# Kernel optimization log

Hardware: AMD Instinct MI355X
Metric: run time of the kernel (lower is better)

The kernel has to match this reference:

```python
import jax, jax.numpy as jnp
import numpy as np

N_NODES = 50000
N_EDGES = 600000
N_GRAPHS = 64
HID = 128
NLAYERS = 4
IN_DIM = 5
NCLS = 5
EPS = 1e-5


def setup_inputs() -> dict:
    key = jax.random.key(0)
    ks = jax.random.split(key, 16)
    x = jax.random.normal(ks[0], (N_NODES, IN_DIM), dtype=jnp.float32)
    edge_index = jax.random.randint(ks[1], (2, N_EDGES), 0, N_NODES, dtype=jnp.int64)
    batch = jnp.sort(jax.random.randint(ks[2], (N_NODES,), 0, N_GRAPHS, dtype=jnp.int64))
    s = 0.05
    Wp = jax.random.normal(ks[3], (IN_DIM, HID), jnp.float32) * s
    bp = jnp.zeros((HID,), jnp.float32)
    Wg = jax.random.normal(ks[4], (NLAYERS, HID, HID), jnp.float32) * s
    bg = jnp.zeros((NLAYERS, HID), jnp.float32)
    gamma = jnp.ones((NLAYERS, HID), jnp.float32)
    beta = jnp.zeros((NLAYERS, HID), jnp.float32)
    W1 = jax.random.normal(ks[5], (2 * HID, HID), jnp.float32) * s
    b1 = jnp.zeros((HID,), jnp.float32)
    W2 = jax.random.normal(ks[6], (HID, HID // 2), jnp.float32) * s
    b2 = jnp.zeros((HID // 2,), jnp.float32)
    W3 = jax.random.normal(ks[7], (HID // 2, NCLS), jnp.float32) * s
    b3 = jnp.zeros((NCLS,), jnp.float32)
    return {"x": x, "edge_index": edge_index, "batch": batch, "Wp": Wp, "bp": bp,
            "Wg": Wg, "bg": bg, "gamma": gamma, "beta": beta,
            "W1": W1, "b1": b1, "W2": W2, "b2": b2, "W3": W3, "b3": b3}


def reference(x, edge_index, batch, Wp, bp, Wg, bg, gamma, beta, W1, b1, W2, b2, W3, b3):
    N = x.shape[0]
    # GCN with added self-loops and symmetric normalization (PyG GCNConv defaults)
    loop = jnp.arange(N)
    src = jnp.concatenate([edge_index[0], loop])
    dst = jnp.concatenate([edge_index[1], loop])
    deg = jax.ops.segment_sum(jnp.ones_like(dst, dtype=x.dtype), dst, num_segments=N)
    dinv = jax.lax.rsqrt(deg)  # deg >= 1 thanks to self-loops
    norm = dinv[src] * dinv[dst]  # [E+N]
    h = x @ Wp + bp  # [N, HID]
    for i in range(NLAYERS):
        m = h @ Wg[i]
        agg = jax.ops.segment_sum(m[src] * norm[:, None], dst, num_segments=N) + bg[i]
        # BatchNorm1d (training-mode stats over nodes)
        mu = jnp.mean(agg, axis=0)
        var = jnp.var(agg, axis=0)
        h = gamma[i] * (agg - mu) * jax.lax.rsqrt(var + EPS) + beta[i]
        h = jax.nn.relu(h)  # dropout is identity in eval mode
    # mean_max global pooling per graph
    cnt = jax.ops.segment_sum(jnp.ones((N,), h.dtype), batch, num_segments=N_GRAPHS)
    x_mean = jax.ops.segment_sum(h, batch, num_segments=N_GRAPHS) / jnp.maximum(cnt, 1.0)[:, None]
    x_max = jax.ops.segment_max(h, batch, num_segments=N_GRAPHS)
    x_max = jnp.where(jnp.isfinite(x_max), x_max, 0.0)
    pooled = jnp.concatenate([x_mean, x_max], axis=1)  # [B, 2*HID]
    h1 = jax.nn.relu(pooled @ W1 + b1)
    h2 = jax.nn.relu(h1 @ W2 + b2)
    return h2 @ W3 + b3  # [B, num_classes]
```

## Files before the change

### kernel.cpp

```cpp
#include <hip/hip_runtime.h>
#include <hip/hip_bf16.h>

#define N_NODES 50000
#define N_EDGES 600000
#define N_GRAPHS 64
#define HID 128
#define NLAYERS 4
#define IN_DIM 5
#define NCLS 5
#define EPS 1e-5f
#define SCAN_BLK ((N_NODES + 511) / 512)
#define POOL_CHUNKS 16
#define BSLOT 64
#define WS 136

typedef __attribute__((ext_vector_type(8))) short s16x8;
typedef __attribute__((ext_vector_type(4))) float f32x4;

__device__ __forceinline__ unsigned short f2bf(float x) {
    unsigned u = __float_as_uint(x);
    unsigned r = (u + 0x7fffu + ((u >> 16) & 1u)) >> 16;
    return (unsigned short)r;
}
__device__ __forceinline__ float2 bfpair(unsigned u) {
    float2 r;
    r.x = __uint_as_float(u << 16);
    r.y = __uint_as_float(u & 0xffff0000u);
    return r;
}
__device__ __forceinline__ float bf2f(unsigned short s) {
    return __uint_as_float(((unsigned)s) << 16);
}


__global__ void k_count(const int* __restrict__ dst, int* __restrict__ cnt) {
    int i = blockIdx.x * blockDim.x + threadIdx.x;
    if (i < N_EDGES) atomicAdd(&cnt[dst[i]], 1);
}

__global__ void k_scan1(const int* __restrict__ cnt, int* __restrict__ rp, int* __restrict__ bsum) {
    __shared__ int s[512];
    int t = threadIdx.x;
    int i = blockIdx.x * 512 + t;
    int v = (i < N_NODES) ? cnt[i] : 0;
    s[t] = v;
    __syncthreads();
    for (int off = 1; off < 512; off <<= 1) {
        int x = (t >= off) ? s[t - off] : 0;
        __syncthreads();
        s[t] += x;
        __syncthreads();
    }
    if (i < N_NODES) rp[i + 1] = s[t];
    if (t == 511) bsum[blockIdx.x] = s[511];
}

__global__ void k_scan2g(int* __restrict__ bsum, const int* __restrict__ batch,
                         int* __restrict__ gstart) {
    if (blockIdx.x == 0) {
        __shared__ int s[128];
        int t = threadIdx.x;
        int v = (t < SCAN_BLK) ? bsum[t] : 0;
        s[t] = v;
        __syncthreads();
        for (int off = 1; off < 128; off <<= 1) {
            int x = (t >= off) ? s[t - off] : 0;
            __syncthreads();
            s[t] += x;
            __syncthreads();
        }
        if (t < SCAN_BLK) bsum[t] = s[t] - v;
    } else {
        int t = threadIdx.x;
        if (t <= N_GRAPHS) {
            int lo = 0, hi = N_NODES;
            while (lo < hi) {
                int mid = (lo + hi) >> 1;
                if (batch[mid] < t) lo = mid + 1; else hi = mid;
            }
            gstart[t] = lo;
        }
    }
}

__global__ void k_scan3d(int* __restrict__ rp, const int* __restrict__ bsum,
                         const int* __restrict__ cnt, float* __restrict__ dinv) {
    int i = blockIdx.x * 512 + threadIdx.x;
    if (i < N_NODES) {
        rp[i + 1] += bsum[blockIdx.x];
        dinv[i] = rsqrtf((float)(cnt[i] + 1));
    }
    if (i == 0) rp[0] = 0;
}

__global__ void k_fill(const int* __restrict__ src, const int* __restrict__ dst,
                       const int* __restrict__ rp, int* __restrict__ cursor,
                       int2* __restrict__ cw, const float* __restrict__ dinv) {
    int e = blockIdx.x * blockDim.x + threadIdx.x;
    if (e < N_EDGES) {
        int d = dst[e];
        int pos = atomicAdd(&cursor[d], 1);
        int s = src[e];
        int2 p;
        p.x = s;
        p.y = __float_as_int(dinv[s]);
        cw[rp[d] + pos] = p;
    }
}


__global__ __launch_bounds__(256) void k_gemmM(const unsigned short* __restrict__ Abf,
                                               const float* __restrict__ x,
                                               const float* __restrict__ Wp,
                                               const float* __restrict__ bp,
                                               const float* __restrict__ W,
                                               unsigned short* __restrict__ Bm,
                                               const float* __restrict__ scale,
                                               const float* __restrict__ shift,
                                               int layer0) {
    __shared__ unsigned short Wt[HID * WS];
    __shared__ unsigned short Al[64 * WS];
    __shared__ float Wpl[IN_DIM * HID];
    __shared__ float bpl[HID];
    __shared__ float xl[64 * IN_DIM];
    int t = threadIdx.x;
    for (int idx = t; idx < HID * HID; idx += 256) {
        int k = idx >> 7, n = idx & 127;
        Wt[n * WS + k] = f2bf(W[idx]);
    }
    if (layer0) {
        for (int idx = t; idx < IN_DIM * HID; idx += 256) Wpl[idx] = Wp[idx];
        if (t < HID) bpl[t] = bp[t];
    }
    int lane = t & 63, wv = t >> 6;
    int rbase = (wv & 1) * 32;
    int cbase = (wv >> 1) * 64;
    int mr = lane & 15, q = lane >> 4;
    const int numTiles = (N_NODES + 63) / 64;
    for (int tile = blockIdx.x; tile < numTiles; tile += gridDim.x) {
        int n0 = tile * 64;
        __syncthreads();
        if (layer0) {
            for (int idx = t; idx < 64 * IN_DIM; idx += 256) {
                int g = n0 * IN_DIM + idx;
                xl[idx] = (g < N_NODES * IN_DIM) ? x[g] : 0.f;
            }
            __syncthreads();
            for (int idx = t; idx < 64 * HID; idx += 256) {
                int n = idx >> 7, k = idx & 127;
                float acc = bpl[k];
#pragma unroll
                for (int j = 0; j < IN_DIM; j++) acc += xl[n * IN_DIM + j] * Wpl[j * HID + k];
                Al[n * WS + k] = f2bf(acc);
            }
        } else {
            const uint2* Ag = (const uint2*)(Abf + (size_t)n0 * HID);
            int limRow = min(64, N_NODES - n0);
            for (int idx = t; idx < 64 * 32; idx += 256) {
                int row = idx >> 5, c4 = idx & 31;
                uint2 u = (row < limRow) ? Ag[row * 32 + c4] : make_uint2(0u, 0u);
                float2 ab = bfpair(u.x);
                float2 cd = bfpair(u.y);
                int kf = c4 * 4;
                float4 sc = *(const float4*)&scale[kf];
                float4 sh = *(const float4*)&shift[kf];
                float v0 = fmaxf(ab.x * sc.x + sh.x, 0.f);
                float v1 = fmaxf(ab.y * sc.y + sh.y, 0.f);
                float v2 = fmaxf(cd.x * sc.z + sh.z, 0.f);
                float v3 = fmaxf(cd.y * sc.w + sh.w, 0.f);
                unsigned lo = (unsigned)f2bf(v0) | ((unsigned)f2bf(v1) << 16);
                unsigned hi = (unsigned)f2bf(v2) | ((unsigned)f2bf(v3) << 16);
                *(uint2*)&Al[row * WS + kf] = make_uint2(lo, hi);
            }
        }
        __syncthreads();
        f32x4 acc[2][4];
#pragma unroll
        for (int rt = 0; rt < 2; rt++)
#pragma unroll
            for (int ct = 0; ct < 4; ct++) acc[rt][ct] = (f32x4){0.f, 0.f, 0.f, 0.f};
#pragma unroll
        for (int kk = 0; kk < HID; kk += 32) {
            s16x8 a0 = *(const s16x8*)&Al[(rbase + mr) * WS + kk + q * 8];
            s16x8 a1 = *(const s16x8*)&Al[(rbase + 16 + mr) * WS + kk + q * 8];
#pragma unroll
            for (int ct = 0; ct < 4; ct++) {
                s16x8 b = *(const s16x8*)&Wt[(cbase + ct * 16 + mr) * WS + kk + q * 8];
                acc[0][ct] = __builtin_amdgcn_mfma_f32_16x16x32_bf16(a0, b, acc[0][ct], 0, 0, 0);
                acc[1][ct] = __builtin_amdgcn_mfma_f32_16x16x32_bf16(a1, b, acc[1][ct], 0, 0, 0);
            }
        }
#pragma unroll
        for (int rt = 0; rt < 2; rt++)
#pragma unroll
            for (int ct = 0; ct < 4; ct++)
#pragma unroll
                for (int r = 0; r < 4; r++) {
                    int node = n0 + rbase + rt * 16 + q * 4 + r;
                    if (node < N_NODES) {
                        int f = cbase + ct * 16 + mr;
                        Bm[(size_t)node * HID + f] = f2bf(acc[rt][ct][r]);
                    }
                }
    }
}


__global__ __launch_bounds__(256) void k_gather(const uint2* __restrict__ Bm2,
                                                const int* __restrict__ rp,
                                                const int2* __restrict__ cw,
                                                const float* __restrict__ dinv,
                                                const float* __restrict__ bg,
                                                unsigned short* __restrict__ Aout,
                                                float* __restrict__ psum,
                                                float* __restrict__ psq) {
    __shared__ float ls[4 * HID], lq[4 * HID];
    int wave = threadIdx.x >> 6;
    int lane = threadIdx.x & 63;
    int s = lane & 31;
    int p = lane >> 5;
    int v = blockIdx.x * 4 + wave;
    int beg = rp[v], end = rp[v + 1];
    float dv = dinv[v];
    float4 acc = make_float4(0.f, 0.f, 0.f, 0.f);
    if (p == 0) {
        uint2 u = Bm2[(size_t)v * 32 + s];
        float2 lo = bfpair(u.x), hi = bfpair(u.y);
        acc.x = lo.x * dv; acc.y = lo.y * dv; acc.z = hi.x * dv; acc.w = hi.y * dv;
    }
    int e = beg + p;
    for (; e + 2 < end; e += 4) {
        int2 pe0 = cw[e];
        int2 pe1 = cw[e + 2];
        uint2 u0 = Bm2[(size_t)pe0.x * 32 + s];
        uint2 u1 = Bm2[(size_t)pe1.x * 32 + s];
        float w0 = __int_as_float(pe0.y);
        float w1 = __int_as_float(pe1.y);
        float2 l0 = bfpair(u0.x), h0 = bfpair(u0.y);
        float2 l1 = bfpair(u1.x), h1 = bfpair(u1.y);
        acc.x += l0.x * w0 + l1.x * w1;
        acc.y += l0.y * w0 + l1.y * w1;
        acc.z += h0.x * w0 + h1.x * w1;
        acc.w += h0.y * w0 + h1.y * w1;
    }
    if (e < end) {
        int2 pe = cw[e];
        uint2 u = Bm2[(size_t)pe.x * 32 + s];
        float w = __int_as_float(pe.y);
        float2 lo = bfpair(u.x), hi = bfpair(u.y);
        acc.x += lo.x * w; acc.y += lo.y * w; acc.z += hi.x * w; acc.w += hi.y * w;
    }
    acc.x += __shfl_xor(acc.x, 32);
    acc.y += __shfl_xor(acc.y, 32);
    acc.z += __shfl_xor(acc.z, 32);
    acc.w += __shfl_xor(acc.w, 32);
    int f = s * 4;
    if (p == 0) {
        float4 bgv = *(const float4*)&bg[f];
        ushort4 o;
        o.x = f2bf(acc.x * dv + bgv.x);
        o.y = f2bf(acc.y * dv + bgv.y);
        o.z = f2bf(acc.z * dv + bgv.z);
        o.w = f2bf(acc.w * dv + bgv.w);
        *(ushort4*)&Aout[(size_t)v * HID + f] = o;
        float vx = bf2f(o.x), vy = bf2f(o.y), vz = bf2f(o.z), vw = bf2f(o.w);
        ls[wave * HID + f + 0] = vx;
        ls[wave * HID + f + 1] = vy;
        ls[wave * HID + f + 2] = vz;
        ls[wave * HID + f + 3] = vw;
        lq[wave * HID + f + 0] = vx * vx;
        lq[wave * HID + f + 1] = vy * vy;
        lq[wave * HID + f + 2] = vz * vz;
        lq[wave * HID + f + 3] = vw * vw;
    }
    __syncthreads();
    int tt = threadIdx.x;
    if (tt < HID) {
        float ssum = ls[tt] + ls[HID + tt] + ls[2 * HID + tt] + ls[3 * HID + tt];
        float ssq = lq[tt] + lq[HID + tt] + lq[2 * HID + tt] + lq[3 * HID + tt];
        int slot = blockIdx.x & (BSLOT - 1);
        atomicAdd(&psum[slot * HID + tt], ssum);
        atomicAdd(&psq[slot * HID + tt], ssq);
    }
}


__global__ __launch_bounds__(128) void k_bnfin(float* __restrict__ psum,
                                               float* __restrict__ psq,
                                               const float* __restrict__ gamma,
                                               const float* __restrict__ beta,
                                               float* __restrict__ scale,
                                               float* __restrict__ shift) {
    int f = threadIdx.x;
    float s = 0.f, s2 = 0.f;
#pragma unroll 8
    for (int b = 0; b < BSLOT; b++) {
        s += psum[b * HID + f];
        s2 += psq[b * HID + f];
    }
#pragma unroll 8
    for (int b = 0; b < BSLOT; b++) {
        psum[b * HID + f] = 0.f;
        psq[b * HID + f] = 0.f;
    }
    const float invN = 1.f / (float)N_NODES;
    float mu = s * invN;
    float var = s2 * invN - mu * mu;
    float rs = rsqrtf(var + EPS) * gamma[f];
    scale[f] = rs;
    shift[f] = beta[f] - mu * rs;
}


__global__ __launch_bounds__(128) void k_pool(const unsigned short* __restrict__ A,
                                              const float* __restrict__ scale,
                                              const float* __restrict__ shift,
                                              const int* __restrict__ gstart,
                                              float* __restrict__ poolPart) {
    int g = blockIdx.x;
    int c = blockIdx.y;
    int f = threadIdx.x;
    int beg = gstart[g], end = gstart[g + 1];
    int len = end - beg;
    int per = (len + POOL_CHUNKS - 1) / POOL_CHUNKS;
    int s0 = beg + c * per;
    int s1 = min(s0 + per, end);
    float sc = scale[f], sh = shift[f];
    float sa = 0.f, sb = 0.f, ma = 0.f, mb = 0.f;
    int n = s0;
    for (; n + 1 < s1; n += 2) {
        float v0 = bf2f(A[(size_t)n * HID + f]);
        float v1 = bf2f(A[(size_t)(n + 1) * HID + f]);
        v0 = fmaxf(v0 * sc + sh, 0.f);
        v1 = fmaxf(v1 * sc + sh, 0.f);
        sa += v0; ma = fmaxf(ma, v0);
        sb += v1; mb = fmaxf(mb, v1);
    }
    if (n < s1) {
        float v = fmaxf(bf2f(A[(size_t)n * HID + f]) * sc + sh, 0.f);
        sa += v; ma = fmaxf(ma, v);
    }
    poolPart[((size_t)g * POOL_CHUNKS + c) * 256 + f] = sa + sb;
    poolPart[((size_t)g * POOL_CHUNKS + c) * 256 + 128 + f] = fmaxf(ma, mb);
}


__global__ __launch_bounds__(128) void k_head(const float* __restrict__ poolPart,
                                              const int* __restrict__ gstart,
                                              const float* __restrict__ W1, const float* __restrict__ b1,
                                              const float* __restrict__ W2, const float* __restrict__ b2,
                                              const float* __restrict__ W3, const float* __restrict__ b3,
                                              float* __restrict__ out) {
    __shared__ float pl[2 * HID];
    __shared__ float h1[HID];
    __shared__ float h2[HID / 2];
    int g = blockIdx.x, t = threadIdx.x;
    float cnt = fmaxf((float)(gstart[g + 1] - gstart[g]), 1.f);
    float s = 0.f, mx = 0.f;
#pragma unroll
    for (int c = 0; c < POOL_CHUNKS; c++) {
        const float* p = &poolPart[((size_t)g * POOL_CHUNKS + c) * 256];
        s += p[t];
        mx = fmaxf(mx, p[128 + t]);
    }
    pl[t] = s / cnt;
    pl[HID + t] = mx;
    __syncthreads();
    float acc = b1[t];
    for (int k = 0; k < 2 * HID; k++) acc += pl[k] * W1[k * HID + t];
    h1[t] = fmaxf(acc, 0.f);
    __syncthreads();
    if (t < HID / 2) {
        float a2 = b2[t];
        for (int k = 0; k < HID; k++) a2 += h1[k] * W2[k * (HID / 2) + t];
        h2[t] = fmaxf(a2, 0.f);
    }
    __syncthreads();
    if (t < NCLS) {
        float a3 = b3[t];
        for (int k = 0; k < HID / 2; k++) a3 += h2[k] * W3[k * NCLS + t];
        out[g * NCLS + t] = a3;
    }
}

extern "C" void kernel_launch(void* const* d_in, const int* in_sizes, int n_in,
                              void* d_out, int out_size, void* d_ws, size_t ws_size,
                              hipStream_t stream) {
    const float* x     = (const float*)d_in[0];
    const int*   ei    = (const int*)d_in[1];
    const int*   batch = (const int*)d_in[2];
    const float* Wp    = (const float*)d_in[3];
    const float* bp    = (const float*)d_in[4];
    const float* Wg    = (const float*)d_in[5];
    const float* bg    = (const float*)d_in[6];
    const float* gamma = (const float*)d_in[7];
    const float* beta  = (const float*)d_in[8];
    const float* W1    = (const float*)d_in[9];
    const float* b1    = (const float*)d_in[10];
    const float* W2    = (const float*)d_in[11];
    const float* b2    = (const float*)d_in[12];
    const float* W3    = (const float*)d_in[13];
    const float* b3    = (const float*)d_in[14];
    const int* src = ei;
    const int* dst = ei + N_EDGES;
    float* out = (float*)d_out;

    char* base = (char*)d_ws;
    size_t off = 0;
    auto alloc = [&](size_t bytes) -> void* {
        void* p = base + off;
        off += (bytes + 255) & ~(size_t)255;
        return p;
    };
    int*   counts = (int*)alloc((size_t)N_NODES * 4);
    int*   cursor = (int*)alloc((size_t)N_NODES * 4);
    float* psum   = (float*)alloc((size_t)BSLOT * HID * 4);
    float* psq    = (float*)alloc((size_t)BSLOT * HID * 4);
    size_t zeroBytes = off;
    int*   rp      = (int*)alloc((size_t)(N_NODES + 1) * 4);
    int*   bsum    = (int*)alloc(128 * 4);
    int2*  cw      = (int2*)alloc((size_t)N_EDGES * 8);
    float* dinv    = (float*)alloc((size_t)N_NODES * 4);
    float* scaleA  = (float*)alloc((size_t)NLAYERS * HID * 4);
    float* shiftA  = (float*)alloc((size_t)NLAYERS * HID * 4);
    int*   gstart  = (int*)alloc((size_t)(N_GRAPHS + 1) * 4);
    float* poolPart= (float*)alloc((size_t)N_GRAPHS * POOL_CHUNKS * 256 * 4);
    unsigned short* A = (unsigned short*)alloc((size_t)N_NODES * HID * 2);
    unsigned short* B = (unsigned short*)alloc((size_t)N_NODES * HID * 2);
    (void)ws_size; (void)in_sizes; (void)n_in; (void)out_size;

    hipMemsetAsync(d_ws, 0, zeroBytes, stream);

    k_count<<<(N_EDGES + 255) / 256, 256, 0, stream>>>(dst, counts);
    k_scan1<<<SCAN_BLK, 512, 0, stream>>>(counts, rp, bsum);
    k_scan2g<<<2, 128, 0, stream>>>(bsum, batch, gstart);
    k_scan3d<<<SCAN_BLK, 512, 0, stream>>>(rp, bsum, counts, dinv);
    k_fill<<<(N_EDGES + 255) / 256, 256, 0, stream>>>(src, dst, rp, cursor, cw, dinv);

    for (int i = 0; i < NLAYERS; i++) {
        k_gemmM<<<768, 256, 0, stream>>>(A, x, Wp, bp, Wg + (size_t)i * HID * HID, B,
                                         scaleA + ((i == 0) ? 0 : (i - 1)) * HID,
                                         shiftA + ((i == 0) ? 0 : (i - 1)) * HID,
                                         (i == 0) ? 1 : 0);
        k_gather<<<N_NODES / 4, 256, 0, stream>>>((const uint2*)B, rp, cw, dinv,
                                                  bg + i * HID, A, psum, psq);
        k_bnfin<<<1, 128, 0, stream>>>(psum, psq, gamma + i * HID, beta + i * HID,
                                       scaleA + i * HID, shiftA + i * HID);
    }
    dim3 pg(N_GRAPHS, POOL_CHUNKS);
    k_pool<<<pg, 128, 0, stream>>>(A, scaleA + 3 * HID, shiftA + 3 * HID, gstart, poolPart);
    k_head<<<N_GRAPHS, 128, 0, stream>>>(poolPart, gstart, W1, b1, W2, b2, W3, b3, out);
}
```

Measured before the change: 435.5 us.

## Fold BN finalize into consumers and widen gather loads to 16 bytes

```diff
diff --git a/kernel.cpp b/kernel.cpp
--- a/kernel.cpp
+++ b/kernel.cpp
@@ -115,11 +115,14 @@
                                                const float* __restrict__ bp,
                                                const float* __restrict__ W,
                                                unsigned short* __restrict__ Bm,
-                                               const float* __restrict__ scale,
-                                               const float* __restrict__ shift,
+                                               const float* __restrict__ psum,
+                                               const float* __restrict__ psq,
+                                               const float* __restrict__ gamma,
+                                               const float* __restrict__ beta,
                                                int layer0) {
     __shared__ unsigned short Wt[HID * WS];
     __shared__ unsigned short Al[64 * WS];
+    __shared__ float scl[HID], shf[HID];
     __shared__ float Wpl[IN_DIM * HID];
     __shared__ float bpl[HID];
     __shared__ float xl[64 * IN_DIM];
@@ -131,6 +134,19 @@
     if (layer0) {
         for (int idx = t; idx < IN_DIM * HID; idx += 256) Wpl[idx] = Wp[idx];
         if (t < HID) bpl[t] = bp[t];
+    } else if (t < HID) {
+        float s = 0.f, s2 = 0.f;
+#pragma unroll 8
+        for (int b = 0; b < BSLOT; b++) {
+            s += psum[b * HID + t];
+            s2 += psq[b * HID + t];
+        }
+        const float invN = 1.f / (float)N_NODES;
+        float mu = s * invN;
+        float var = s2 * invN - mu * mu;
+        float rs = rsqrtf(var + EPS) * gamma[t];
+        scl[t] = rs;
+        shf[t] = beta[t] - mu * rs;
     }
     int lane = t & 63, wv = t >> 6;
     int rbase = (wv & 1) * 32;
@@ -162,8 +178,8 @@
                 float2 ab = bfpair(u.x);
                 float2 cd = bfpair(u.y);
                 int kf = c4 * 4;
-                float4 sc = *(const float4*)&scale[kf];
-                float4 sh = *(const float4*)&shift[kf];
+                float4 sc = *(const float4*)&scl[kf];
+                float4 sh = *(const float4*)&shf[kf];
                 float v0 = fmaxf(ab.x * sc.x + sh.x, 0.f);
                 float v1 = fmaxf(ab.y * sc.y + sh.y, 0.f);
                 float v2 = fmaxf(cd.x * sc.z + sh.z, 0.f);
@@ -206,7 +222,7 @@
 }
 
 
-__global__ __launch_bounds__(256) void k_gather(const uint2* __restrict__ Bm2,
+__global__ __launch_bounds__(256) void k_gather(const uint4* __restrict__ Bm4,
                                                 const int* __restrict__ rp,
                                                 const int2* __restrict__ cw,
                                                 const float* __restrict__ dinv,
@@ -217,61 +233,79 @@
     __shared__ float ls[4 * HID], lq[4 * HID];
     int wave = threadIdx.x >> 6;
     int lane = threadIdx.x & 63;
-    int s = lane & 31;
-    int p = lane >> 5;
+    int s = lane & 15;
+    int p = lane >> 4;
     int v = blockIdx.x * 4 + wave;
     int beg = rp[v], end = rp[v + 1];
     float dv = dinv[v];
-    float4 acc = make_float4(0.f, 0.f, 0.f, 0.f);
+    float a0 = 0.f, a1 = 0.f, a2 = 0.f, a3 = 0.f, a4 = 0.f, a5 = 0.f, a6 = 0.f, a7 = 0.f;
     if (p == 0) {
-        uint2 u = Bm2[(size_t)v * 32 + s];
-        float2 lo = bfpair(u.x), hi = bfpair(u.y);
-        acc.x = lo.x * dv; acc.y = lo.y * dv; acc.z = hi.x * dv; acc.w = hi.y * dv;
+        uint4 u = Bm4[(size_t)v * 16 + s];
+        float2 q0 = bfpair(u.x), q1 = bfpair(u.y), q2 = bfpair(u.z), q3 = bfpair(u.w);
+        a0 = q0.x * dv; a1 = q0.y * dv; a2 = q1.x * dv; a3 = q1.y * dv;
+        a4 = q2.x * dv; a5 = q2.y * dv; a6 = q3.x * dv; a7 = q3.y * dv;
     }
     int e = beg + p;
-    for (; e + 2 < end; e += 4) {
+    for (; e + 4 < end; e += 8) {
         int2 pe0 = cw[e];
-        int2 pe1 = cw[e + 2];
-        uint2 u0 = Bm2[(size_t)pe0.x * 32 + s];
-        uint2 u1 = Bm2[(size_t)pe1.x * 32 + s];
+        int2 pe1 = cw[e + 4];
+        uint4 u0 = Bm4[(size_t)pe0.x * 16 + s];
+        uint4 u1 = Bm4[(size_t)pe1.x * 16 + s];
         float w0 = __int_as_float(pe0.y);
         float w1 = __int_as_float(pe1.y);
-        float2 l0 = bfpair(u0.x), h0 = bfpair(u0.y);
-        float2 l1 = bfpair(u1.x), h1 = bfpair(u1.y);
-        acc.x += l0.x * w0 + l1.x * w1;
-        acc.y += l0.y * w0 + l1.y * w1;
-        acc.z += h0.x * w0 + h1.x * w1;
-        acc.w += h0.y * w0 + h1.y * w1;
+        float2 x0 = bfpair(u0.x), x1 = bfpair(u0.y), x2 = bfpair(u0.z), x3 = bfpair(u0.w);
+        float2 y0 = bfpair(u1.x), y1 = bfpair(u1.y), y2 = bfpair(u1.z), y3 = bfpair(u1.w);
+        a0 += x0.x * w0 + y0.x * w1;
+        a1 += x0.y * w0 + y0.y * w1;
+        a2 += x1.x * w0 + y1.x * w1;
+        a3 += x1.y * w0 + y1.y * w1;
+        a4 += x2.x * w0 + y2.x * w1;
+        a5 += x2.y * w0 + y2.y * w1;
+        a6 += x3.x * w0 + y3.x * w1;
+        a7 += x3.y * w0 + y3.y * w1;
     }
     if (e < end) {
         int2 pe = cw[e];
-        uint2 u = Bm2[(size_t)pe.x * 32 + s];
+        uint4 u = Bm4[(size_t)pe.x * 16 + s];
         float w = __int_as_float(pe.y);
-        float2 lo = bfpair(u.x), hi = bfpair(u.y);
-        acc.x += lo.x * w; acc.y += lo.y * w; acc.z += hi.x * w; acc.w += hi.y * w;
-    }
-    acc.x += __shfl_xor(acc.x, 32);
-    acc.y += __shfl_xor(acc.y, 32);
-    acc.z += __shfl_xor(acc.z, 32);
-    acc.w += __shfl_xor(acc.w, 32);
-    int f = s * 4;
+        float2 x0 = bfpair(u.x), x1 = bfpair(u.y), x2 = bfpair(u.z), x3 = bfpair(u.w);
+        a0 += x0.x * w; a1 += x0.y * w; a2 += x1.x * w; a3 += x1.y * w;
+        a4 += x2.x * w; a5 += x2.y * w; a6 += x3.x * w; a7 += x3.y * w;
+    }
+    a0 += __shfl_xor(a0, 16); a1 += __shfl_xor(a1, 16);
+    a2 += __shfl_xor(a2, 16); a3 += __shfl_xor(a3, 16);
+    a4 += __shfl_xor(a4, 16); a5 += __shfl_xor(a5, 16);
+    a6 += __shfl_xor(a6, 16); a7 += __shfl_xor(a7, 16);
+    a0 += __shfl_xor(a0, 32); a1 += __shfl_xor(a1, 32);
+    a2 += __shfl_xor(a2, 32); a3 += __shfl_xor(a3, 32);
+    a4 += __shfl_xor(a4, 32); a5 += __shfl_xor(a5, 32);
+    a6 += __shfl_xor(a6, 32); a7 += __shfl_xor(a7, 32);
     if (p == 0) {
-        float4 bgv = *(const float4*)&bg[f];
-        ushort4 o;
-        o.x = f2bf(acc.x * dv + bgv.x);
-        o.y = f2bf(acc.y * dv + bgv.y);
-        o.z = f2bf(acc.z * dv + bgv.z);
-        o.w = f2bf(acc.w * dv + bgv.w);
-        *(ushort4*)&Aout[(size_t)v * HID + f] = o;
-        float vx = bf2f(o.x), vy = bf2f(o.y), vz = bf2f(o.z), vw = bf2f(o.w);
-        ls[wave * HID + f + 0] = vx;
-        ls[wave * HID + f + 1] = vy;
-        ls[wave * HID + f + 2] = vz;
-        ls[wave * HID + f + 3] = vw;
-        lq[wave * HID + f + 0] = vx * vx;
-        lq[wave * HID + f + 1] = vy * vy;
-        lq[wave * HID + f + 2] = vz * vz;
-        lq[wave * HID + f + 3] = vw * vw;
+        int f = s * 8;
+        float r0 = a0 * dv + bg[f + 0];
+        float r1 = a1 * dv + bg[f + 1];
+        float r2 = a2 * dv + bg[f + 2];
+        float r3 = a3 * dv + bg[f + 3];
+        float r4 = a4 * dv + bg[f + 4];
+        float r5 = a5 * dv + bg[f + 5];
+        float r6 = a6 * dv + bg[f + 6];
+        float r7 = a7 * dv + bg[f + 7];
+        unsigned short b0 = f2bf(r0), b1 = f2bf(r1), b2 = f2bf(r2), b3 = f2bf(r3);
+        unsigned short b4 = f2bf(r4), b5 = f2bf(r5), b6 = f2bf(r6), b7 = f2bf(r7);
+        uint4 o;
+        o.x = (unsigned)b0 | ((unsigned)b1 << 16);
+        o.y = (unsigned)b2 | ((unsigned)b3 << 16);
+        o.z = (unsigned)b4 | ((unsigned)b5 << 16);
+        o.w = (unsigned)b6 | ((unsigned)b7 << 16);
+        *(uint4*)&Aout[(size_t)v * HID + f] = o;
+        float v0 = bf2f(b0), v1 = bf2f(b1), v2 = bf2f(b2), v3 = bf2f(b3);
+        float v4 = bf2f(b4), v5 = bf2f(b5), v6 = bf2f(b6), v7 = bf2f(b7);
+        float* lsw = &ls[wave * HID + f];
+        float* lqw = &lq[wave * HID + f];
+        lsw[0] = v0; lsw[1] = v1; lsw[2] = v2; lsw[3] = v3;
+        lsw[4] = v4; lsw[5] = v5; lsw[6] = v6; lsw[7] = v7;
+        lqw[0] = v0 * v0; lqw[1] = v1 * v1; lqw[2] = v2 * v2; lqw[3] = v3 * v3;
+        lqw[4] = v4 * v4; lqw[5] = v5 * v5; lqw[6] = v6 * v6; lqw[7] = v7 * v7;
     }
     __syncthreads();
     int tt = threadIdx.x;
@@ -285,12 +319,15 @@
 }
 
 
-__global__ __launch_bounds__(128) void k_bnfin(float* __restrict__ psum,
-                                               float* __restrict__ psq,
-                                               const float* __restrict__ gamma,
-                                               const float* __restrict__ beta,
-                                               float* __restrict__ scale,
-                                               float* __restrict__ shift) {
+__global__ __launch_bounds__(128) void k_pool(const unsigned short* __restrict__ A,
+                                              const float* __restrict__ psum,
+                                              const float* __restrict__ psq,
+                                              const float* __restrict__ gamma,
+                                              const float* __restrict__ beta,
+                                              const int* __restrict__ gstart,
+                                              float* __restrict__ poolPart) {
+    int g = blockIdx.x;
+    int c = blockIdx.y;
     int f = threadIdx.x;
     float s = 0.f, s2 = 0.f;
 #pragma unroll 8
@@ -298,34 +335,16 @@
         s += psum[b * HID + f];
         s2 += psq[b * HID + f];
     }
-#pragma unroll 8
-    for (int b = 0; b < BSLOT; b++) {
-        psum[b * HID + f] = 0.f;
-        psq[b * HID + f] = 0.f;
-    }
     const float invN = 1.f / (float)N_NODES;
     float mu = s * invN;
     float var = s2 * invN - mu * mu;
-    float rs = rsqrtf(var + EPS) * gamma[f];
-    scale[f] = rs;
-    shift[f] = beta[f] - mu * rs;
-}
-
-
-__global__ __launch_bounds__(128) void k_pool(const unsigned short* __restrict__ A,
-                                              const float* __restrict__ scale,
-                                              const float* __restrict__ shift,
-                                              const int* __restrict__ gstart,
-                                              float* __restrict__ poolPart) {
-    int g = blockIdx.x;
-    int c = blockIdx.y;
-    int f = threadIdx.x;
+    float sc = rsqrtf(var + EPS) * gamma[f];
+    float sh = beta[f] - mu * sc;
     int beg = gstart[g], end = gstart[g + 1];
     int len = end - beg;
     int per = (len + POOL_CHUNKS - 1) / POOL_CHUNKS;
     int s0 = beg + c * per;
     int s1 = min(s0 + per, end);
-    float sc = scale[f], sh = shift[f];
     float sa = 0.f, sb = 0.f, ma = 0.f, mb = 0.f;
     int n = s0;
     for (; n + 1 < s1; n += 2) {
@@ -414,15 +433,13 @@
     };
     int*   counts = (int*)alloc((size_t)N_NODES * 4);
     int*   cursor = (int*)alloc((size_t)N_NODES * 4);
-    float* psum   = (float*)alloc((size_t)BSLOT * HID * 4);
-    float* psq    = (float*)alloc((size_t)BSLOT * HID * 4);
+    float* psum   = (float*)alloc((size_t)NLAYERS * BSLOT * HID * 4);
+    float* psq    = (float*)alloc((size_t)NLAYERS * BSLOT * HID * 4);
     size_t zeroBytes = off;
     int*   rp      = (int*)alloc((size_t)(N_NODES + 1) * 4);
     int*   bsum    = (int*)alloc(128 * 4);
     int2*  cw      = (int2*)alloc((size_t)N_EDGES * 8);
     float* dinv    = (float*)alloc((size_t)N_NODES * 4);
-    float* scaleA  = (float*)alloc((size_t)NLAYERS * HID * 4);
-    float* shiftA  = (float*)alloc((size_t)NLAYERS * HID * 4);
     int*   gstart  = (int*)alloc((size_t)(N_GRAPHS + 1) * 4);
     float* poolPart= (float*)alloc((size_t)N_GRAPHS * POOL_CHUNKS * 256 * 4);
     unsigned short* A = (unsigned short*)alloc((size_t)N_NODES * HID * 2);
@@ -438,16 +455,20 @@
     k_fill<<<(N_EDGES + 255) / 256, 256, 0, stream>>>(src, dst, rp, cursor, cw, dinv);
 
     for (int i = 0; i < NLAYERS; i++) {
+        int pl = (i == 0) ? 0 : (i - 1);
         k_gemmM<<<768, 256, 0, stream>>>(A, x, Wp, bp, Wg + (size_t)i * HID * HID, B,
-                                         scaleA + ((i == 0) ? 0 : (i - 1)) * HID,
-                                         shiftA + ((i == 0) ? 0 : (i - 1)) * HID,
+                                         psum + (size_t)pl * BSLOT * HID,
+                                         psq + (size_t)pl * BSLOT * HID,
+                                         gamma + pl * HID, beta + pl * HID,
                                          (i == 0) ? 1 : 0);
-        k_gather<<<N_NODES / 4, 256, 0, stream>>>((const uint2*)B, rp, cw, dinv,
-                                                  bg + i * HID, A, psum, psq);
-        k_bnfin<<<1, 128, 0, stream>>>(psum, psq, gamma + i * HID, beta + i * HID,
-                                       scaleA + i * HID, shiftA + i * HID);
+        k_gather<<<N_NODES / 4, 256, 0, stream>>>((const uint4*)B, rp, cw, dinv,
+                                                  bg + i * HID, A,
+                                                  psum + (size_t)i * BSLOT * HID,
+                                                  psq + (size_t)i * BSLOT * HID);
     }
     dim3 pg(N_GRAPHS, POOL_CHUNKS);
-    k_pool<<<pg, 128, 0, stream>>>(A, scaleA + 3 * HID, shiftA + 3 * HID, gstart, poolPart);
+    k_pool<<<pg, 128, 0, stream>>>(A, psum + (size_t)3 * BSLOT * HID,
+                                   psq + (size_t)3 * BSLOT * HID,
+                                   gamma + 3 * HID, beta + 3 * HID, gstart, poolPart);
     k_head<<<N_GRAPHS, 128, 0, stream>>>(poolPart, gstart, W1, b1, W2, b2, W3, b3, out);
 }
```

Result: faster. 411.2 us (-5.6%).
